# Optimization experiments

Measured on AMD Instinct MI355X. Metric: run time of the kernel, lower is better.

Reference implementation:

```python
import jax, jax.numpy as jnp
import numpy as np

N, F, E = 50000, 256, 1000000
H1, D1, D2 = 4, 32, 64
NUM_NEW = 10000


def setup_inputs() -> dict:
    key = jax.random.key(0)
    ks = jax.random.split(key, 12)
    return {
        "x": jax.random.normal(ks[0], (N, F), jnp.float32),
        "src": jax.random.randint(ks[1], (E,), 0, N, jnp.int32),
        "dst": jax.random.randint(ks[2], (E,), 0, N, jnp.int32),
        "W1": jax.random.normal(ks[3], (F, H1 * D1), jnp.float32) * 0.05,
        "att_src1": jax.random.normal(ks[4], (H1, D1), jnp.float32) * 0.1,
        "att_dst1": jax.random.normal(ks[5], (H1, D1), jnp.float32) * 0.1,
        "b1": jax.random.normal(ks[6], (H1 * D1,), jnp.float32) * 0.02,
        "W2": jax.random.normal(ks[7], (H1 * D1, D2), jnp.float32) * 0.05,
        "att_src2": jax.random.normal(ks[8], (1, D2), jnp.float32) * 0.1,
        "att_dst2": jax.random.normal(ks[9], (1, D2), jnp.float32) * 0.1,
        "b2": jax.random.normal(ks[10], (D2,), jnp.float32) * 0.02,
        "num_new": NUM_NEW,
    }


def _gat_conv(x, src, dst, W, a_src, a_dst, b, concat):
    # x: [N, Fin]; W: [Fin, H*D]; a_src/a_dst: [H, D]
    n = x.shape[0]
    h, d = a_src.shape
    hx = (x @ W).reshape(n, h, d)                       # [N, H, D]
    alpha_s = jnp.einsum("nhd,hd->nh", hx, a_src)       # [N, H]
    alpha_d = jnp.einsum("nhd,hd->nh", hx, a_dst)
    e = jax.nn.leaky_relu(alpha_s[src] + alpha_d[dst], 0.2)  # [E, H]
    # segment softmax over destination nodes
    e_max = jax.ops.segment_max(e, dst, num_segments=n)      # [N, H]
    e_exp = jnp.exp(e - e_max[dst])
    denom = jax.ops.segment_sum(e_exp, dst, num_segments=n)
    alpha = e_exp / (denom[dst] + 1e-16)                     # [E, H]
    msg = hx[src] * alpha[:, :, None]                        # [E, H, D]
    out = jax.ops.segment_sum(msg, dst, num_segments=n)      # [N, H, D]
    out = out.reshape(n, h * d) if concat else out.mean(axis=1)
    return out + b


def reference(x, src, dst, W1, att_src1, att_dst1, b1, W2, att_src2, att_dst2, b2, num_new):
    x1 = jax.nn.elu(_gat_conv(x, src, dst, W1, att_src1, att_dst1, b1, True))
    x2 = _gat_conv(x1, src, dst, W2, att_src2, att_dst2, b2, False)
    return x2[-num_new:]
```

## Files before the change

kernel.cpp:

```cpp
#include <hip/hip_runtime.h>
#include <hip/hip_fp16.h>
#include <math.h>

#define F_IN   256
#define C1     128
#define H1N    4
#define D2N    64

#define SCAN_T    256
#define SCAN_TILE 512

#define BK2 32

#define NBLK_P 256
#define NBUK_MAX 256

typedef __attribute__((ext_vector_type(8))) _Float16 f16x8;
typedef __attribute__((ext_vector_type(4))) float    f32x4;

__global__ void w1_transpose(const float* __restrict__ W1, __half* __restrict__ W1T) {
    int c = blockIdx.x;
    for (int k = threadIdx.x; k < F_IN; k += blockDim.x)
        W1T[(size_t)c * F_IN + k] = __float2half(W1[(size_t)k * C1 + c]);
}

__global__ void part_hist(const int* __restrict__ dst, int* __restrict__ bcounts,
                          int E, int chunk, int nbuk) {
    __shared__ int h[NBUK_MAX];
    for (int t = threadIdx.x; t < nbuk; t += blockDim.x) h[t] = 0;
    __syncthreads();
    int lo = blockIdx.x * chunk, hi = min(lo + chunk, E);
    for (int i = lo + threadIdx.x; i < hi; i += blockDim.x)
        atomicAdd(&h[dst[i] >> 8], 1);
    __syncthreads();
    for (int t = threadIdx.x; t < nbuk; t += blockDim.x)
        bcounts[(size_t)t * NBLK_P + blockIdx.x] = h[t];
}

__global__ void part_scatter(const int* __restrict__ src, const int* __restrict__ dst,
                             const int* __restrict__ bbase, int2* __restrict__ pedge,
                             int E, int chunk, int nbuk) {
    __shared__ int cur[NBUK_MAX];
    for (int t = threadIdx.x; t < nbuk; t += blockDim.x)
        cur[t] = bbase[(size_t)t * NBLK_P + blockIdx.x];
    __syncthreads();
    int lo = blockIdx.x * chunk, hi = min(lo + chunk, E);
    for (int i = lo + threadIdx.x; i < hi; i += blockDim.x) {
        int d = dst[i];
        int p = atomicAdd(&cur[d >> 8], 1);
        pedge[p] = make_int2(src[i], d);
    }
}

__global__ __launch_bounds__(256) void part_csr(
        const int2* __restrict__ pedge, const int* __restrict__ bbase,
        int* __restrict__ offsets, int* __restrict__ edge_src,
        int N, int E, int nbuk) {
    __shared__ int fcnt[256];
    __shared__ int fsc[256];
    int b = blockIdx.x;
    int t = threadIdx.x;
    int ebeg = bbase[(size_t)b * NBLK_P];
    int eend = (b + 1 < nbuk) ? bbase[(size_t)(b + 1) * NBLK_P] : E;
    int nbase = b << 8;
    fcnt[t] = 0;
    __syncthreads();
    for (int i = ebeg + t; i < eend; i += 256)
        atomicAdd(&fcnt[pedge[i].y - nbase], 1);
    __syncthreads();
    int v = fcnt[t];
    fsc[t] = v;
    __syncthreads();
    for (int off = 1; off < 256; off <<= 1) {
        int u = (t >= off) ? fsc[t - off] : 0;
        __syncthreads();
        fsc[t] += u;
        __syncthreads();
    }
    int goff = ebeg + fsc[t] - v;
    int node = nbase + t;
    if (node < N) offsets[node] = goff;
    if (b == nbuk - 1 && t == 0) offsets[N] = E;
    __syncthreads();
    fcnt[t] = goff;
    __syncthreads();
    for (int i = ebeg + t; i < eend; i += 256) {
        int2 e = pedge[i];
        int p = atomicAdd(&fcnt[e.y - nbase], 1);
        edge_src[p] = e.x;
    }
}

__global__ __launch_bounds__(256) void gemm1_kernel(
        const float* __restrict__ x, const __half* __restrict__ W1T,
        const float* __restrict__ attS, const float* __restrict__ attD,
        __half* __restrict__ hx1h, float* __restrict__ as1, float* __restrict__ ad1,
        int N) {
    __shared__ __half xh[64][40];

    int tid = threadIdx.x;
    int wv  = tid >> 6;
    int l   = tid & 63;
    int n0  = blockIdx.x * 64;

    f32x4 acc[8];
#pragma unroll
    for (int t = 0; t < 8; ++t) acc[t] = (f32x4){0.f, 0.f, 0.f, 0.f};

    int srow = tid >> 2;
    int skg  = (tid & 3) * 8;
    int xrow = n0 + srow; if (xrow >= N) xrow = N - 1;
    const float* xptr = x + (size_t)xrow * F_IN;

    int arow = wv * 16 + (l & 15);
    int akk  = (l >> 4) * 8;
    int bcol = l & 15;
    int bkk  = (l >> 4) * 8;

    for (int s = 0; s < 8; ++s) {
        int k0 = s * 32;
        float4 a0 = *(const float4*)(xptr + k0 + skg);
        float4 a1 = *(const float4*)(xptr + k0 + skg + 4);
        __syncthreads();
        __half2* dp = (__half2*)&xh[srow][skg];
        dp[0] = __floats2half2_rn(a0.x, a0.y);
        dp[1] = __floats2half2_rn(a0.z, a0.w);
        dp[2] = __floats2half2_rn(a1.x, a1.y);
        dp[3] = __floats2half2_rn(a1.z, a1.w);
        __syncthreads();
        f16x8 af = *reinterpret_cast<const f16x8*>(&xh[arow][akk]);
#pragma unroll
        for (int t = 0; t < 8; ++t) {
            f16x8 bf = *reinterpret_cast<const f16x8*>(
                W1T + (size_t)(16 * t + bcol) * F_IN + k0 + bkk);
            acc[t] = __builtin_amdgcn_mfma_f32_16x16x32_f16(af, bf, acc[t], 0, 0, 0);
        }
    }

    float aS[8], aD[8];
#pragma unroll
    for (int t = 0; t < 8; ++t) {
        aS[t] = attS[16 * t + bcol];
        aD[t] = attD[16 * t + bcol];
    }
#pragma unroll
    for (int r = 0; r < 4; ++r) {
        int n = n0 + wv * 16 + 4 * (l >> 4) + r;
        float ts[4], td[4];
#pragma unroll
        for (int h = 0; h < 4; ++h) {
            ts[h] = acc[2 * h][r] * aS[2 * h] + acc[2 * h + 1][r] * aS[2 * h + 1];
            td[h] = acc[2 * h][r] * aD[2 * h] + acc[2 * h + 1][r] * aD[2 * h + 1];
        }
#pragma unroll
        for (int off = 1; off <= 8; off <<= 1)
#pragma unroll
            for (int h = 0; h < 4; ++h) {
                ts[h] += __shfl_xor(ts[h], off, 64);
                td[h] += __shfl_xor(td[h], off, 64);
            }
        if (n < N) {
#pragma unroll
            for (int t = 0; t < 8; ++t)
                hx1h[(size_t)n * C1 + 16 * t + bcol] = __float2half(acc[t][r]);
            if (bcol == 0) {
#pragma unroll
                for (int h = 0; h < 4; ++h) {
                    as1[n * H1N + h] = ts[h];
                    ad1[n * H1N + h] = td[h];
                }
            }
        }
    }
}

__global__ void scan_partial(const int* __restrict__ counts, int* __restrict__ tilesums, int N) {
    __shared__ int red[SCAN_T];
    int t  = threadIdx.x;
    int i0 = blockIdx.x * SCAN_TILE + 2 * t;
    int s = 0;
    if (i0     < N) s += counts[i0];
    if (i0 + 1 < N) s += counts[i0 + 1];
    red[t] = s;
    __syncthreads();
    for (int off = SCAN_T / 2; off > 0; off >>= 1) {
        if (t < off) red[t] += red[t + off];
        __syncthreads();
    }
    if (t == 0) tilesums[blockIdx.x] = red[0];
}

__global__ void scan_tops(const int* __restrict__ tilesums, int* __restrict__ tilebase, int ntiles) {
    __shared__ int sh[SCAN_T];
    int t = threadIdx.x;
    int v = (t < ntiles) ? tilesums[t] : 0;
    sh[t] = v;
    __syncthreads();
    for (int off = 1; off < SCAN_T; off <<= 1) {
        int u = (t >= off) ? sh[t - off] : 0;
        __syncthreads();
        sh[t] += u;
        __syncthreads();
    }
    tilebase[t] = sh[t] - v;
}

__global__ void scan_final(const int* __restrict__ counts, const int* __restrict__ tilebase,
                           int* __restrict__ base, int N, int E) {
    __shared__ int sh[SCAN_T];
    int t  = threadIdx.x;
    int i0 = blockIdx.x * SCAN_TILE + 2 * t;
    int a   = (i0     < N) ? counts[i0]     : 0;
    int b   = (i0 + 1 < N) ? counts[i0 + 1] : 0;
    int tot = a + b;
    sh[t] = tot;
    __syncthreads();
    for (int off = 1; off < SCAN_T; off <<= 1) {
        int u = (t >= off) ? sh[t - off] : 0;
        __syncthreads();
        sh[t] += u;
        __syncthreads();
    }
    int excl = sh[t] - tot + tilebase[blockIdx.x];
    if (i0 < N)     base[i0]     = excl;
    if (i0 + 1 < N) base[i0 + 1] = excl + a;
    if (blockIdx.x == 0 && t == 0) base[N] = E;
}

__global__ void agg1_kernel(const int* __restrict__ edge_src, const int* __restrict__ offsets,
                            const float* __restrict__ as1, const float* __restrict__ ad1,
                            const __half* __restrict__ hx1h, const float* __restrict__ b1,
                            float* __restrict__ x1, int N) {
    __shared__ int   ssh[4][64];
    __shared__ float esh[4][64][4];
    int wid  = threadIdx.x >> 6;
    int n    = (blockIdx.x * blockDim.x + threadIdx.x) >> 6;
    int lane = threadIdx.x & 63;
    if (n >= N) return;
    int hsel = lane >> 4;
    const float4 ad4 = *(const float4*)(ad1 + 4 * n);
    int beg = offsets[n], end = offsets[n + 1];

    float den[4] = {0.f, 0.f, 0.f, 0.f};
    float acc0 = 0.f, acc1 = 0.f;

    for (int cb = beg; cb < end; cb += 64) {
        int j = cb + lane;
        bool valid = j < end;
        int s = valid ? edge_src[j] : 0;
        float e0 = 0.f, e1 = 0.f, e2 = 0.f, e3 = 0.f;
        if (valid) {
            const float4 a4 = *(const float4*)(as1 + 4 * s);
            float v0 = a4.x + ad4.x, v1 = a4.y + ad4.y;
            float v2 = a4.z + ad4.z, v3 = a4.w + ad4.w;
            v0 = v0 > 0.f ? v0 : 0.2f * v0;
            v1 = v1 > 0.f ? v1 : 0.2f * v1;
            v2 = v2 > 0.f ? v2 : 0.2f * v2;
            v3 = v3 > 0.f ? v3 : 0.2f * v3;
            e0 = __expf(v0); e1 = __expf(v1);
            e2 = __expf(v2); e3 = __expf(v3);
            den[0] += e0; den[1] += e1; den[2] += e2; den[3] += e3;
        }
        ssh[wid][lane] = s;
        *(float4*)&esh[wid][lane][0] = make_float4(e0, e1, e2, e3);

        int cnt = min(64, end - cb);
#pragma unroll 4
        for (int jj = 0; jj < cnt; ++jj) {
            int   sj = ssh[wid][jj];
            float w  = esh[wid][jj][hsel];
            const __half2* hr = (const __half2*)(hx1h + (size_t)sj * C1);
            float2 vf = __half22float2(hr[lane]);
            acc0 += w * vf.x;
            acc1 += w * vf.y;
        }
    }

#pragma unroll
    for (int off = 32; off > 0; off >>= 1)
#pragma unroll
        for (int h = 0; h < 4; ++h) den[h] += __shfl_xor(den[h], off, 64);

    float d = lane < 16 ? den[0] : lane < 32 ? den[1] : lane < 48 ? den[2] : den[3];
    float inv = 1.f / (d + 1e-16f);
    float2 bv = *(const float2*)(b1 + 2 * lane);
    float o0 = acc0 * inv + bv.x;
    float o1 = acc1 * inv + bv.y;
    o0 = o0 > 0.f ? o0 : (__expf(o0) - 1.f);
    o1 = o1 > 0.f ? o1 : (__expf(o1) - 1.f);
    *(float2*)&x1[(size_t)n * C1 + 2 * lane] = make_float2(o0, o1);
}

__global__ __launch_bounds__(256) void gemm2_kernel(
        const float* __restrict__ x1, const float* __restrict__ W2,
        const float* __restrict__ attS, const float* __restrict__ attD,
        float* __restrict__ hx2, float* __restrict__ as2, float* __restrict__ ad2,
        int N) {
    __shared__ float xT[BK2][64 + 4];
    __shared__ float ws2[BK2][D2N];

    int tid = threadIdx.x;
    int tx  = tid & 15;
    int ty  = tid >> 4;
    int n0  = blockIdx.x * 64;

    float acc[4][4];
#pragma unroll
    for (int r = 0; r < 4; ++r)
#pragma unroll
        for (int c = 0; c < 4; ++c) acc[r][c] = 0.f;

    int lr = tid >> 2;
    int lk = (tid & 3) * 4;
    int xrow = n0 + lr; if (xrow >= N) xrow = N - 1;
    const float* xptr = x1 + (size_t)xrow * C1;
    int kw = tid >> 4;
    int cw = tx * 4;

    for (int k0 = 0; k0 < C1; k0 += BK2) {
        float4 a0 = *(const float4*)(xptr + k0 + lk);
        float4 a1 = *(const float4*)(xptr + k0 + lk + 16);
        float4 w0 = *(const float4*)(W2 + (size_t)(k0 + kw     ) * D2N + cw);
        float4 w1 = *(const float4*)(W2 + (size_t)(k0 + kw + 16) * D2N + cw);
        __syncthreads();
        xT[lk + 0][lr] = a0.x; xT[lk + 1][lr] = a0.y;
        xT[lk + 2][lr] = a0.z; xT[lk + 3][lr] = a0.w;
        xT[lk + 16][lr] = a1.x; xT[lk + 17][lr] = a1.y;
        xT[lk + 18][lr] = a1.z; xT[lk + 19][lr] = a1.w;
        *(float4*)&ws2[kw     ][cw] = w0;
        *(float4*)&ws2[kw + 16][cw] = w1;
        __syncthreads();
#pragma unroll
        for (int k = 0; k < BK2; ++k) {
            float4 xa = *(const float4*)&xT[k][ty * 4];
            float4 wv = *(const float4*)&ws2[k][tx * 4];
            float xr[4] = {xa.x, xa.y, xa.z, xa.w};
            float wc[4] = {wv.x, wv.y, wv.z, wv.w};
#pragma unroll
            for (int r = 0; r < 4; ++r)
#pragma unroll
                for (int c = 0; c < 4; ++c) acc[r][c] += xr[r] * wc[c];
        }
    }

    const float4 asv = *(const float4*)(attS + tx * 4);
    const float4 adv = *(const float4*)(attD + tx * 4);
#pragma unroll
    for (int r = 0; r < 4; ++r) {
        int n = n0 + ty * 4 + r;
        float ts = acc[r][0] * asv.x + acc[r][1] * asv.y + acc[r][2] * asv.z + acc[r][3] * asv.w;
        float td = acc[r][0] * adv.x + acc[r][1] * adv.y + acc[r][2] * adv.z + acc[r][3] * adv.w;
        ts += __shfl_xor(ts, 1); td += __shfl_xor(td, 1);
        ts += __shfl_xor(ts, 2); td += __shfl_xor(td, 2);
        ts += __shfl_xor(ts, 4); td += __shfl_xor(td, 4);
        ts += __shfl_xor(ts, 8); td += __shfl_xor(td, 8);
        if (n < N) {
            *(float4*)&hx2[(size_t)n * D2N + tx * 4] =
                make_float4(acc[r][0], acc[r][1], acc[r][2], acc[r][3]);
            if (tx == 0) { as2[n] = ts; ad2[n] = td; }
        }
    }
}

__global__ void agg2_kernel(const int* __restrict__ edge_src, const int* __restrict__ offsets,
                            const float* __restrict__ as2, const float* __restrict__ ad2,
                            const float* __restrict__ hx2, const float* __restrict__ b2,
                            float* __restrict__ out, int N, int num_new) {
    __shared__ int   ssh[4][64];
    __shared__ float esh[4][64];
    int wid  = threadIdx.x >> 6;
    int w    = (blockIdx.x * blockDim.x + threadIdx.x) >> 6;
    int lane = threadIdx.x & 63;
    if (w >= num_new) return;
    int n = N - num_new + w;
    float adn = ad2[n];
    int beg = offsets[n], end = offsets[n + 1];

    float den = 0.f, acc = 0.f;
    for (int cb = beg; cb < end; cb += 64) {
        int j = cb + lane;
        bool valid = j < end;
        int s = valid ? edge_src[j] : 0;
        float e = 0.f;
        if (valid) {
            float v = as2[s] + adn;
            v = v > 0.f ? v : 0.2f * v;
            e = __expf(v);
            den += e;
        }
        ssh[wid][lane] = s;
        esh[wid][lane] = e;

        int cnt = min(64, end - cb);
#pragma unroll 4
        for (int jj = 0; jj < cnt; ++jj) {
            int   sj = ssh[wid][jj];
            float wj = esh[wid][jj];
            acc += wj * hx2[(size_t)sj * D2N + lane];
        }
    }
#pragma unroll
    for (int off = 32; off > 0; off >>= 1) den += __shfl_xor(den, off, 64);
    out[(size_t)w * D2N + lane] = acc / (den + 1e-16f) + b2[lane];
}

extern "C" void kernel_launch(void* const* d_in, const int* in_sizes, int n_in,
                              void* d_out, int out_size, void* d_ws, size_t ws_size,
                              hipStream_t stream) {
    const float* x      = (const float*)d_in[0];
    const int*   src    = (const int*)d_in[1];
    const int*   dst    = (const int*)d_in[2];
    const float* W1     = (const float*)d_in[3];
    const float* attS1  = (const float*)d_in[4];
    const float* attD1  = (const float*)d_in[5];
    const float* b1     = (const float*)d_in[6];
    const float* W2     = (const float*)d_in[7];
    const float* attS2  = (const float*)d_in[8];
    const float* attD2  = (const float*)d_in[9];
    const float* b2     = (const float*)d_in[10];

    const int N = in_sizes[0] / F_IN;
    const int E = in_sizes[1];
    const int num_new = out_size / D2N;
    const int ngemm  = (N + 63) / 64;
    const int nbuk   = (N + 255) >> 8;
    const int M      = nbuk * NBLK_P;
    const int ntilesM = (M + SCAN_TILE - 1) / SCAN_TILE;
    const int chunk  = (E + NBLK_P - 1) / NBLK_P;

    __half* hx1h = (__half*)d_ws;
    float* x1  = (float*)(hx1h + (size_t)N * C1);
    float* hx2 = x1  + (size_t)N * C1;
    float* as1 = hx2 + (size_t)N * D2N;
    float* ad1 = as1 + (size_t)N * H1N;
    float* as2 = ad1 + (size_t)N * H1N;
    float* ad2 = as2 + N;
    int* bcounts  = (int*)(ad2 + N);
    int* bbase    = bcounts + M;
    int* offsets  = bbase + M + 1;
    int* tilesums = offsets + N + 1;
    int* tilebase = tilesums + 256;
    int* edge_src = tilebase + 256;
    int2* pedge   = (int2*)(edge_src + E);
    __half* W1T   = (__half*)(pedge + E);

    float* out = (float*)d_out;

    hipLaunchKernelGGL(w1_transpose, dim3(C1), dim3(256), 0, stream, W1, W1T);
    hipLaunchKernelGGL(part_hist, dim3(NBLK_P), dim3(256), 0, stream,
                       dst, bcounts, E, chunk, nbuk);
    hipLaunchKernelGGL(gemm1_kernel, dim3(ngemm), dim3(256), 0, stream,
                       x, W1T, attS1, attD1, hx1h, as1, ad1, N);
    hipLaunchKernelGGL(scan_partial, dim3(ntilesM), dim3(SCAN_T), 0, stream, bcounts, tilesums, M);
    hipLaunchKernelGGL(scan_tops, dim3(1), dim3(SCAN_T), 0, stream, tilesums, tilebase, ntilesM);
    hipLaunchKernelGGL(scan_final, dim3(ntilesM), dim3(SCAN_T), 0, stream,
                       bcounts, tilebase, bbase, M, E);
    hipLaunchKernelGGL(part_scatter, dim3(NBLK_P), dim3(256), 0, stream,
                       src, dst, bbase, pedge, E, chunk, nbuk);
    hipLaunchKernelGGL(part_csr, dim3(nbuk), dim3(256), 0, stream,
                       pedge, bbase, offsets, edge_src, N, E, nbuk);
    hipLaunchKernelGGL(agg1_kernel, dim3((N + 3) / 4), dim3(256), 0, stream,
                       edge_src, offsets, as1, ad1, hx1h, b1, x1, N);
    hipLaunchKernelGGL(gemm2_kernel, dim3((N + 63) / 64), dim3(256), 0, stream,
                       x1, W2, attS2, attD2, hx2, as2, ad2, N);
    hipLaunchKernelGGL(agg2_kernel, dim3((num_new + 3) / 4), dim3(256), 0, stream,
                       edge_src, offsets, as2, ad2, hx2, b2, out, N, num_new);
}
```

Measured before the change: 164.1 us.

## Store layer-1 output and layer-2 features in fp16; fuse histogram into gemm1 launch

After: 151.5 us. 7.7% less time.

```diff
diff --git a/kernel.cpp b/kernel.cpp
--- a/kernel.cpp
+++ b/kernel.cpp
@@ -24,17 +24,103 @@
         W1T[(size_t)c * F_IN + k] = __float2half(W1[(size_t)k * C1 + c]);
 }
 
-__global__ void part_hist(const int* __restrict__ dst, int* __restrict__ bcounts,
-                          int E, int chunk, int nbuk) {
-    __shared__ int h[NBUK_MAX];
-    for (int t = threadIdx.x; t < nbuk; t += blockDim.x) h[t] = 0;
-    __syncthreads();
-    int lo = blockIdx.x * chunk, hi = min(lo + chunk, E);
-    for (int i = lo + threadIdx.x; i < hi; i += blockDim.x)
-        atomicAdd(&h[dst[i] >> 8], 1);
-    __syncthreads();
-    for (int t = threadIdx.x; t < nbuk; t += blockDim.x)
-        bcounts[(size_t)t * NBLK_P + blockIdx.x] = h[t];
+__global__ __launch_bounds__(256) void gemm1_hist_kernel(
+        const float* __restrict__ x, const __half* __restrict__ W1T,
+        const float* __restrict__ attS, const float* __restrict__ attD,
+        __half* __restrict__ hx1h, float* __restrict__ as1, float* __restrict__ ad1,
+        int N,
+        const int* __restrict__ dst, int* __restrict__ bcounts,
+        int E, int chunk, int nbuk, int ngemm) {
+    if ((int)blockIdx.x >= ngemm) {
+        __shared__ int h[NBUK_MAX];
+        int b = blockIdx.x - ngemm;
+        for (int t = threadIdx.x; t < nbuk; t += blockDim.x) h[t] = 0;
+        __syncthreads();
+        int lo = b * chunk, hi = min(lo + chunk, E);
+        for (int i = lo + threadIdx.x; i < hi; i += blockDim.x)
+            atomicAdd(&h[dst[i] >> 8], 1);
+        __syncthreads();
+        for (int t = threadIdx.x; t < nbuk; t += blockDim.x)
+            bcounts[(size_t)t * NBLK_P + b] = h[t];
+        return;
+    }
+
+    __shared__ __half xh[64][40];
+
+    int tid = threadIdx.x;
+    int wv  = tid >> 6;
+    int l   = tid & 63;
+    int n0  = blockIdx.x * 64;
+
+    f32x4 acc[8];
+#pragma unroll
+    for (int t = 0; t < 8; ++t) acc[t] = (f32x4){0.f, 0.f, 0.f, 0.f};
+
+    int srow = tid >> 2;
+    int skg  = (tid & 3) * 8;
+    int xrow = n0 + srow; if (xrow >= N) xrow = N - 1;
+    const float* xptr = x + (size_t)xrow * F_IN;
+
+    int arow = wv * 16 + (l & 15);
+    int akk  = (l >> 4) * 8;
+    int bcol = l & 15;
+    int bkk  = (l >> 4) * 8;
+
+    for (int s = 0; s < 8; ++s) {
+        int k0 = s * 32;
+        float4 a0 = *(const float4*)(xptr + k0 + skg);
+        float4 a1 = *(const float4*)(xptr + k0 + skg + 4);
+        __syncthreads();
+        __half2* dp = (__half2*)&xh[srow][skg];
+        dp[0] = __floats2half2_rn(a0.x, a0.y);
+        dp[1] = __floats2half2_rn(a0.z, a0.w);
+        dp[2] = __floats2half2_rn(a1.x, a1.y);
+        dp[3] = __floats2half2_rn(a1.z, a1.w);
+        __syncthreads();
+        f16x8 af = *reinterpret_cast<const f16x8*>(&xh[arow][akk]);
+#pragma unroll
+        for (int t = 0; t < 8; ++t) {
+            f16x8 bf = *reinterpret_cast<const f16x8*>(
+                W1T + (size_t)(16 * t + bcol) * F_IN + k0 + bkk);
+            acc[t] = __builtin_amdgcn_mfma_f32_16x16x32_f16(af, bf, acc[t], 0, 0, 0);
+        }
+    }
+
+    float aS[8], aD[8];
+#pragma unroll
+    for (int t = 0; t < 8; ++t) {
+        aS[t] = attS[16 * t + bcol];
+        aD[t] = attD[16 * t + bcol];
+    }
+#pragma unroll
+    for (int r = 0; r < 4; ++r) {
+        int n = n0 + wv * 16 + 4 * (l >> 4) + r;
+        float ts[4], td[4];
+#pragma unroll
+        for (int h = 0; h < 4; ++h) {
+            ts[h] = acc[2 * h][r] * aS[2 * h] + acc[2 * h + 1][r] * aS[2 * h + 1];
+            td[h] = acc[2 * h][r] * aD[2 * h] + acc[2 * h + 1][r] * aD[2 * h + 1];
+        }
+#pragma unroll
+        for (int off = 1; off <= 8; off <<= 1)
+#pragma unroll
+            for (int h = 0; h < 4; ++h) {
+                ts[h] += __shfl_xor(ts[h], off, 64);
+                td[h] += __shfl_xor(td[h], off, 64);
+            }
+        if (n < N) {
+#pragma unroll
+            for (int t = 0; t < 8; ++t)
+                hx1h[(size_t)n * C1 + 16 * t + bcol] = __float2half(acc[t][r]);
+            if (bcol == 0) {
+#pragma unroll
+                for (int h = 0; h < 4; ++h) {
+                    as1[n * H1N + h] = ts[h];
+                    ad1[n * H1N + h] = td[h];
+                }
+            }
+        }
+    }
 }
 
 __global__ void part_scatter(const int* __restrict__ src, const int* __restrict__ dst,
@@ -91,89 +177,6 @@
     }
 }
 
-__global__ __launch_bounds__(256) void gemm1_kernel(
-        const float* __restrict__ x, const __half* __restrict__ W1T,
-        const float* __restrict__ attS, const float* __restrict__ attD,
-        __half* __restrict__ hx1h, float* __restrict__ as1, float* __restrict__ ad1,
-        int N) {
-    __shared__ __half xh[64][40];
-
-    int tid = threadIdx.x;
-    int wv  = tid >> 6;
-    int l   = tid & 63;
-    int n0  = blockIdx.x * 64;
-
-    f32x4 acc[8];
-#pragma unroll
-    for (int t = 0; t < 8; ++t) acc[t] = (f32x4){0.f, 0.f, 0.f, 0.f};
-
-    int srow = tid >> 2;
-    int skg  = (tid & 3) * 8;
-    int xrow = n0 + srow; if (xrow >= N) xrow = N - 1;
-    const float* xptr = x + (size_t)xrow * F_IN;
-
-    int arow = wv * 16 + (l & 15);
-    int akk  = (l >> 4) * 8;
-    int bcol = l & 15;
-    int bkk  = (l >> 4) * 8;
-
-    for (int s = 0; s < 8; ++s) {
-        int k0 = s * 32;
-        float4 a0 = *(const float4*)(xptr + k0 + skg);
-        float4 a1 = *(const float4*)(xptr + k0 + skg + 4);
-        __syncthreads();
-        __half2* dp = (__half2*)&xh[srow][skg];
-        dp[0] = __floats2half2_rn(a0.x, a0.y);
-        dp[1] = __floats2half2_rn(a0.z, a0.w);
-        dp[2] = __floats2half2_rn(a1.x, a1.y);
-        dp[3] = __floats2half2_rn(a1.z, a1.w);
-        __syncthreads();
-        f16x8 af = *reinterpret_cast<const f16x8*>(&xh[arow][akk]);
-#pragma unroll
-        for (int t = 0; t < 8; ++t) {
-            f16x8 bf = *reinterpret_cast<const f16x8*>(
-                W1T + (size_t)(16 * t + bcol) * F_IN + k0 + bkk);
-            acc[t] = __builtin_amdgcn_mfma_f32_16x16x32_f16(af, bf, acc[t], 0, 0, 0);
-        }
-    }
-
-    float aS[8], aD[8];
-#pragma unroll
-    for (int t = 0; t < 8; ++t) {
-        aS[t] = attS[16 * t + bcol];
-        aD[t] = attD[16 * t + bcol];
-    }
-#pragma unroll
-    for (int r = 0; r < 4; ++r) {
-        int n = n0 + wv * 16 + 4 * (l >> 4) + r;
-        float ts[4], td[4];
-#pragma unroll
-        for (int h = 0; h < 4; ++h) {
-            ts[h] = acc[2 * h][r] * aS[2 * h] + acc[2 * h + 1][r] * aS[2 * h + 1];
-            td[h] = acc[2 * h][r] * aD[2 * h] + acc[2 * h + 1][r] * aD[2 * h + 1];
-        }
-#pragma unroll
-        for (int off = 1; off <= 8; off <<= 1)
-#pragma unroll
-            for (int h = 0; h < 4; ++h) {
-                ts[h] += __shfl_xor(ts[h], off, 64);
-                td[h] += __shfl_xor(td[h], off, 64);
-            }
-        if (n < N) {
-#pragma unroll
-            for (int t = 0; t < 8; ++t)
-                hx1h[(size_t)n * C1 + 16 * t + bcol] = __float2half(acc[t][r]);
-            if (bcol == 0) {
-#pragma unroll
-                for (int h = 0; h < 4; ++h) {
-                    as1[n * H1N + h] = ts[h];
-                    ad1[n * H1N + h] = td[h];
-                }
-            }
-        }
-    }
-}
-
 __global__ void scan_partial(const int* __restrict__ counts, int* __restrict__ tilesums, int N) {
     __shared__ int red[SCAN_T];
     int t  = threadIdx.x;
@@ -230,7 +233,7 @@
 __global__ void agg1_kernel(const int* __restrict__ edge_src, const int* __restrict__ offsets,
                             const float* __restrict__ as1, const float* __restrict__ ad1,
                             const __half* __restrict__ hx1h, const float* __restrict__ b1,
-                            float* __restrict__ x1, int N) {
+                            __half* __restrict__ x1h, int N) {
     __shared__ int   ssh[4][64];
     __shared__ float esh[4][64][4];
     int wid  = threadIdx.x >> 6;
@@ -288,13 +291,13 @@
     float o1 = acc1 * inv + bv.y;
     o0 = o0 > 0.f ? o0 : (__expf(o0) - 1.f);
     o1 = o1 > 0.f ? o1 : (__expf(o1) - 1.f);
-    *(float2*)&x1[(size_t)n * C1 + 2 * lane] = make_float2(o0, o1);
+    *(__half2*)&x1h[(size_t)n * C1 + 2 * lane] = __floats2half2_rn(o0, o1);
 }
 
 __global__ __launch_bounds__(256) void gemm2_kernel(
-        const float* __restrict__ x1, const float* __restrict__ W2,
+        const __half* __restrict__ x1h, const float* __restrict__ W2,
         const float* __restrict__ attS, const float* __restrict__ attD,
-        float* __restrict__ hx2, float* __restrict__ as2, float* __restrict__ ad2,
+        __half* __restrict__ hx2h, float* __restrict__ as2, float* __restrict__ ad2,
         int N) {
     __shared__ float xT[BK2][64 + 4];
     __shared__ float ws2[BK2][D2N];
@@ -311,22 +314,19 @@
         for (int c = 0; c < 4; ++c) acc[r][c] = 0.f;
 
     int lr = tid >> 2;
-    int lk = (tid & 3) * 4;
+    int lk = (tid & 3) * 8;
     int xrow = n0 + lr; if (xrow >= N) xrow = N - 1;
-    const float* xptr = x1 + (size_t)xrow * C1;
+    const __half* xptr = x1h + (size_t)xrow * C1;
     int kw = tid >> 4;
     int cw = tx * 4;
 
     for (int k0 = 0; k0 < C1; k0 += BK2) {
-        float4 a0 = *(const float4*)(xptr + k0 + lk);
-        float4 a1 = *(const float4*)(xptr + k0 + lk + 16);
+        f16x8 a = *reinterpret_cast<const f16x8*>(xptr + k0 + lk);
         float4 w0 = *(const float4*)(W2 + (size_t)(k0 + kw     ) * D2N + cw);
         float4 w1 = *(const float4*)(W2 + (size_t)(k0 + kw + 16) * D2N + cw);
         __syncthreads();
-        xT[lk + 0][lr] = a0.x; xT[lk + 1][lr] = a0.y;
-        xT[lk + 2][lr] = a0.z; xT[lk + 3][lr] = a0.w;
-        xT[lk + 16][lr] = a1.x; xT[lk + 17][lr] = a1.y;
-        xT[lk + 18][lr] = a1.z; xT[lk + 19][lr] = a1.w;
+#pragma unroll
+        for (int j = 0; j < 8; ++j) xT[lk + j][lr] = (float)a[j];
         *(float4*)&ws2[kw     ][cw] = w0;
         *(float4*)&ws2[kw + 16][cw] = w1;
         __syncthreads();
@@ -355,8 +355,8 @@
         ts += __shfl_xor(ts, 4); td += __shfl_xor(td, 4);
         ts += __shfl_xor(ts, 8); td += __shfl_xor(td, 8);
         if (n < N) {
-            *(float4*)&hx2[(size_t)n * D2N + tx * 4] =
-                make_float4(acc[r][0], acc[r][1], acc[r][2], acc[r][3]);
+            *(__half2*)&hx2h[(size_t)n * D2N + tx * 4]     = __floats2half2_rn(acc[r][0], acc[r][1]);
+            *(__half2*)&hx2h[(size_t)n * D2N + tx * 4 + 2] = __floats2half2_rn(acc[r][2], acc[r][3]);
             if (tx == 0) { as2[n] = ts; ad2[n] = td; }
         }
     }
@@ -364,7 +364,7 @@
 
 __global__ void agg2_kernel(const int* __restrict__ edge_src, const int* __restrict__ offsets,
                             const float* __restrict__ as2, const float* __restrict__ ad2,
-                            const float* __restrict__ hx2, const float* __restrict__ b2,
+                            const __half* __restrict__ hx2h, const float* __restrict__ b2,
                             float* __restrict__ out, int N, int num_new) {
     __shared__ int   ssh[4][64];
     __shared__ float esh[4][64];
@@ -396,7 +396,7 @@
         for (int jj = 0; jj < cnt; ++jj) {
             int   sj = ssh[wid][jj];
             float wj = esh[wid][jj];
-            acc += wj * hx2[(size_t)sj * D2N + lane];
+            acc += wj * __half2float(hx2h[(size_t)sj * D2N + lane]);
         }
     }
 #pragma unroll
@@ -429,9 +429,9 @@
     const int chunk  = (E + NBLK_P - 1) / NBLK_P;
 
     __half* hx1h = (__half*)d_ws;
-    float* x1  = (float*)(hx1h + (size_t)N * C1);
-    float* hx2 = x1  + (size_t)N * C1;
-    float* as1 = hx2 + (size_t)N * D2N;
+    __half* x1h  = hx1h + (size_t)N * C1;
+    __half* hx2h = x1h  + (size_t)N * C1;
+    float* as1 = (float*)(hx2h + (size_t)N * D2N);
     float* ad1 = as1 + (size_t)N * H1N;
     float* as2 = ad1 + (size_t)N * H1N;
     float* ad2 = as2 + N;
@@ -447,10 +447,9 @@
     float* out = (float*)d_out;
 
     hipLaunchKernelGGL(w1_transpose, dim3(C1), dim3(256), 0, stream, W1, W1T);
-    hipLaunchKernelGGL(part_hist, dim3(NBLK_P), dim3(256), 0, stream,
-                       dst, bcounts, E, chunk, nbuk);
-    hipLaunchKernelGGL(gemm1_kernel, dim3(ngemm), dim3(256), 0, stream,
-                       x, W1T, attS1, attD1, hx1h, as1, ad1, N);
+    hipLaunchKernelGGL(gemm1_hist_kernel, dim3(ngemm + NBLK_P), dim3(256), 0, stream,
+                       x, W1T, attS1, attD1, hx1h, as1, ad1, N,
+                       dst, bcounts, E, chunk, nbuk, ngemm);
     hipLaunchKernelGGL(scan_partial, dim3(ntilesM), dim3(SCAN_T), 0, stream, bcounts, tilesums, M);
     hipLaunchKernelGGL(scan_tops, dim3(1), dim3(SCAN_T), 0, stream, tilesums, tilebase, ntilesM);
     hipLaunchKernelGGL(scan_final, dim3(ntilesM), dim3(SCAN_T), 0, stream,
@@ -460,9 +459,9 @@
     hipLaunchKernelGGL(part_csr, dim3(nbuk), dim3(256), 0, stream,
                        pedge, bbase, offsets, edge_src, N, E, nbuk);
     hipLaunchKernelGGL(agg1_kernel, dim3((N + 3) / 4), dim3(256), 0, stream,
-                       edge_src, offsets, as1, ad1, hx1h, b1, x1, N);
+                       edge_src, offsets, as1, ad1, hx1h, b1, x1h, N);
     hipLaunchKernelGGL(gemm2_kernel, dim3((N + 63) / 64), dim3(256), 0, stream,
-                       x1, W2, attS2, attD2, hx2, as2, ad2, N);
+                       x1h, W2, attS2, attD2, hx2h, as2, ad2, N);
     hipLaunchKernelGGL(agg2_kernel, dim3((num_new + 3) / 4), dim3(256), 0, stream,
-                       edge_src, offsets, as2, ad2, hx2, b2, out, N, num_new);
-}
+                       edge_src, offsets, as2, ad2, hx2h, b2, out, N, num_new);
+}
```
